# Performance work log

Hardware: AMD Instinct MI355X
Metric: run time of the kernel (lower is better)

The kernel has to match this reference:

```python
import jax, jax.numpy as jnp
import numpy as np

B, S, D = 4, 1024, 512
H, HD, M = 8, 64, 2
EPS = 1e-5


def setup_inputs() -> dict:
    key = jax.random.key(0)
    ks = jax.random.split(key, 8)
    scale = 0.02
    x = jax.random.normal(ks[0], (B, S, D), dtype=jnp.float32)
    Wq = jax.random.normal(ks[1], (D, D), dtype=jnp.float32) * scale
    Wk = jax.random.normal(ks[2], (D, D), dtype=jnp.float32) * scale
    Wv = jax.random.normal(ks[3], (D, D), dtype=jnp.float32) * scale
    Wo = jax.random.normal(ks[4], (D, D), dtype=jnp.float32) * scale
    bo = jnp.zeros((D,), dtype=jnp.float32)
    Wg = jax.random.normal(ks[5], (H * (2 + M), D), dtype=jnp.float32) * scale
    bg = jnp.zeros((H * (2 + M),), dtype=jnp.float32)
    init_decays = jnp.array([0.95, 0.8], dtype=jnp.float32)
    logit = jnp.log(init_decays / (1.0 - init_decays))
    logit_alphas = jnp.tile(logit[None, :], (H, 1))  # [H, M]
    ln_w = jnp.ones((D,), dtype=jnp.float32)
    ln_b = jnp.zeros((D,), dtype=jnp.float32)
    return {"x": x, "Wq": Wq, "Wk": Wk, "Wv": Wv, "Wo": Wo, "bo": bo,
            "Wg": Wg, "bg": bg, "logit_alphas": logit_alphas,
            "ln_w": ln_w, "ln_b": ln_b}


def _rope(x):
    # x: [B, S, H, HD] interleaved rotary
    half = HD // 2
    inv_freq = 1.0 / (10000.0 ** (jnp.arange(half, dtype=jnp.float32) / half))
    t = jnp.arange(S, dtype=jnp.float32)
    freqs = t[:, None] * inv_freq[None, :]            # [S, half]
    cos = jnp.cos(freqs)[None, :, None, :]            # [1, S, 1, half]
    sin = jnp.sin(freqs)[None, :, None, :]
    x1, x2 = x[..., ::2], x[..., 1::2]
    o1 = x1 * cos - x2 * sin
    o2 = x1 * sin + x2 * cos
    return jnp.stack((o1, o2), axis=-1).reshape(x.shape)


def _forward(x, Wq, Wk, Wv, Wo, bo, Wg, bg, logit_alphas, ln_w, ln_b):
    residual = x
    q = (x @ Wq.T).reshape(B, S, H, HD)
    k = (x @ Wk.T).reshape(B, S, H, HD)
    v = (x @ Wv.T).reshape(B, S, H, HD)
    q = _rope(q)
    k = _rope(k)

    gates = (x @ Wg.T + bg).reshape(B, S, H, 2 + M)
    g_f = jax.nn.sigmoid(gates[..., 0])               # [B, S, H]
    g_u = jax.nn.sigmoid(gates[..., 1])               # [B, S, H]
    w_mix = jax.nn.softmax(gates[..., 2:], axis=-1)   # [B, S, H, M]
    alphas = jax.nn.sigmoid(logit_alphas)             # [H, M]

    # time-major for scan
    qs = jnp.moveaxis(q, 1, 0)       # [S, B, H, HD]
    ks = jnp.moveaxis(k, 1, 0)
    vs = jnp.moveaxis(v, 1, 0)
    gfs = jnp.moveaxis(g_f, 1, 0)    # [S, B, H]
    gus = jnp.moveaxis(g_u, 1, 0)
    wms = jnp.moveaxis(w_mix, 1, 0)  # [S, B, H, M]

    state0 = jnp.zeros((B, H, M, HD, HD), dtype=x.dtype)

    def step(state, inp):
        qt, kt, vt, gf, gu, wt = inp
        retain = alphas[None, :, :] * gf[:, :, None]           # [B, H, M]
        write_w = wt * gu[..., None]                           # [B, H, M]
        outer = jnp.einsum('bhd,bhe->bhde', kt, vt)            # [B, H, HD, HD]
        state = (state * retain[..., None, None]
                 + outer[:, :, None, :, :] * write_w[..., None, None])
        S_read = jnp.einsum('bhmde,bhm->bhde', state, wt)      # [B, H, HD, HD]
        o = jnp.einsum('bhd,bhde->bhe', qt, S_read)            # [B, H, HD]
        return state, o

    _, outs = jax.lax.scan(step, state0, (qs, ks, vs, gfs, gus, wms))
    out = jnp.moveaxis(outs, 0, 1).reshape(B, S, H * HD)
    out = out @ Wo.T + bo
    y = residual + out
    mu = jnp.mean(y, axis=-1, keepdims=True)
    var = jnp.mean(jnp.square(y - mu), axis=-1, keepdims=True)
    return (y - mu) / jnp.sqrt(var + EPS) * ln_w + ln_b


def reference(x, Wq, Wk, Wv, Wo, bo, Wg, bg, logit_alphas, ln_w, ln_b):
    return _forward(x, Wq, Wk, Wv, Wo, bo, Wg, bg, logit_alphas, ln_w, ln_b)
```

## Files before the change

kernel.cpp:

```cpp
#include <hip/hip_runtime.h>
#include <hip/hip_bf16.h>
#include <math.h>

#define B_  4
#define S_  1024
#define D_  512
#define H_  8
#define HD_ 64
#define EPS_ 1e-5f

typedef __attribute__((ext_vector_type(8))) short  bf16x8;
typedef __attribute__((ext_vector_type(4))) short  bf16x4;
typedef __attribute__((ext_vector_type(4))) float  f32x4;

#define MFMA16(a, b, c) __builtin_amdgcn_mfma_f32_16x16x32_bf16((a), (b), (c), 0, 0, 0)

#define GLOAD16(gp, lp) __builtin_amdgcn_global_load_lds( \
    (const __attribute__((address_space(1))) unsigned int*)(gp), \
    (__attribute__((address_space(3))) unsigned int*)(lp), 16, 0, 0)

__device__ __forceinline__ float bf2f(short u) {
    union { unsigned int i; float f; } v;
    v.i = ((unsigned int)(unsigned short)u) << 16;
    return v.f;
}
__device__ __forceinline__ short f2bf(float f) {
    __hip_bfloat16 h = __float2bfloat16(f);
    return *reinterpret_cast<short*>(&h);
}

__global__ __launch_bounds__(256) void convert_inputs(
    const float* __restrict__ x,
    const float* __restrict__ Wq, const float* __restrict__ Wk,
    const float* __restrict__ Wv, const float* __restrict__ Wg,
    const float* __restrict__ Wo,
    short* __restrict__ xbf, short* __restrict__ Wcat, short* __restrict__ Wobf,
    float2* __restrict__ rope)
{
    const int id = blockIdx.x * 256 + threadIdx.x;
    if (id < 262144) {
        const size_t e = (size_t)id * 8;
        float4 v0 = *(const float4*)(x + e);
        float4 v1 = *(const float4*)(x + e + 4);
        bf16x8 o = { f2bf(v0.x), f2bf(v0.y), f2bf(v0.z), f2bf(v0.w),
                     f2bf(v1.x), f2bf(v1.y), f2bf(v1.z), f2bf(v1.w) };
        *(bf16x8*)(xbf + e) = o;
    } else if (id < 368640) {
        const int i2 = id - 262144;
        const int row = i2 >> 6;
        const int c8 = (i2 & 63) * 8;
        const float* s = nullptr;
        if (row < 512)       s = Wq + (size_t)row * 512 + c8;
        else if (row < 1024) s = Wk + (size_t)(row - 512) * 512 + c8;
        else if (row < 1536) s = Wv + (size_t)(row - 1024) * 512 + c8;
        else if (row < 1568) s = Wg + (size_t)(row - 1536) * 512 + c8;
        bf16x8 o = (bf16x8)0;
        if (s) {
            float4 v0 = *(const float4*)(s);
            float4 v1 = *(const float4*)(s + 4);
            o = bf16x8{ f2bf(v0.x), f2bf(v0.y), f2bf(v0.z), f2bf(v0.w),
                        f2bf(v1.x), f2bf(v1.y), f2bf(v1.z), f2bf(v1.w) };
        }
        *(bf16x8*)(Wcat + (size_t)row * 512 + c8) = o;
    } else if (id < 401408) {
        const int i3 = id - 368640;
        const size_t e = (size_t)i3 * 8;
        float4 v0 = *(const float4*)(Wo + e);
        float4 v1 = *(const float4*)(Wo + e + 4);
        bf16x8 o = { f2bf(v0.x), f2bf(v0.y), f2bf(v0.z), f2bf(v0.w),
                     f2bf(v1.x), f2bf(v1.y), f2bf(v1.z), f2bf(v1.w) };
        *(bf16x8*)(Wobf + e) = o;
    } else {
        const int i4 = id - 401408;
        const int s = i4 >> 5, i = i4 & 31;
        const float inv = exp2f(-(float)i * (13.287712379549449f / 32.0f));
        float sn, cs;
        sincosf((float)s * inv, &sn, &cs);
        rope[i4] = make_float2(cs, sn);
    }
}

__global__ __launch_bounds__(256) void mfma_proj(
    const short* __restrict__ Abf, const short* __restrict__ Wcat,
    const float2* __restrict__ rope,
    short* __restrict__ Qbf, short* __restrict__ Kbf,
    short* __restrict__ Vbf, float* __restrict__ Graw)
{
    __shared__ __align__(16) short lds[32768];

    const int p = blockIdx.x;
    const int xcd = p & 7, slot = p >> 3;
    const int by = xcd + 8 * (slot / 13);
    const int bx = slot % 13;
    const int n0 = bx * 128, m0 = by * 128;

    const int tid = threadIdx.x;
    const int lane = tid & 63, wave = tid >> 6;
    const int lrow = lane & 15, lgrp = lane >> 4;
    const int wr = wave >> 1, wc = wave & 1;
    const int srl = lane >> 3;
    const int scs = (lane & 7) * 8;

    f32x4 acc[4][4];
    #pragma unroll
    for (int i = 0; i < 4; ++i)
        #pragma unroll
        for (int j = 0; j < 4; ++j) acc[i][j] = (f32x4)0.f;

    #define PROJ_STAGE(buf, kt)  {                                            \
        short* dA = lds + (buf) * 16384;                                      \
        short* dB = dA + 8192;                                                \
        _Pragma("unroll")                                                     \
        for (int i = 0; i < 4; ++i) {                                         \
            const int chunk = i * 4 + wave;                                   \
            const int r = chunk * 8 + srl;                                    \
            GLOAD16(Abf  + (size_t)(m0 + r) * 512 + (kt) + scs, dA + chunk * 512); \
            GLOAD16(Wcat + (size_t)(n0 + r) * 512 + (kt) + scs, dB + chunk * 512); \
        } }

    PROJ_STAGE(0, 0);
    __syncthreads();
    int cur = 0;
    for (int step = 0; step < 8; ++step) {
        if (step < 7) PROJ_STAGE(cur ^ 1, (step + 1) * 64);
        const short* sA = lds + cur * 16384;
        const short* sB = sA + 8192;
        #pragma unroll
        for (int kk = 0; kk < 2; ++kk) {
            const int kb = kk * 32 + lgrp * 8;
            bf16x8 af[4], bfr[4];
            #pragma unroll
            for (int mi = 0; mi < 4; ++mi)
                af[mi] = *(const bf16x8*)&sA[(wr * 64 + mi * 16 + lrow) * 64 + kb];
            #pragma unroll
            for (int ni = 0; ni < 4; ++ni)
                bfr[ni] = *(const bf16x8*)&sB[(wc * 64 + ni * 16 + lrow) * 64 + kb];
            #pragma unroll
            for (int mi = 0; mi < 4; ++mi)
                #pragma unroll
                for (int ni = 0; ni < 4; ++ni)
                    acc[mi][ni] = MFMA16(af[mi], bfr[ni], acc[mi][ni]);
        }
        __syncthreads();
        cur ^= 1;
    }
    #undef PROJ_STAGE

    if (n0 < 1536) {
        short* stg = lds;
        #pragma unroll
        for (int mi = 0; mi < 4; ++mi)
            #pragma unroll
            for (int ni = 0; ni < 4; ++ni)
                #pragma unroll
                for (int j = 0; j < 4; ++j) {
                    const int rl = wr * 64 + mi * 16 + lgrp * 4 + j;
                    const int cl = wc * 64 + ni * 16 + lrow;
                    stg[rl * 136 + cl] = f2bf(acc[mi][ni][j]);
                }
        __syncthreads();
        short* dst; int dstoff; bool roped;
        if (n0 < 512)       { dst = Qbf; dstoff = n0;        roped = true;  }
        else if (n0 < 1024) { dst = Kbf; dstoff = n0 - 512;  roped = true;  }
        else                { dst = Vbf; dstoff = n0 - 1024; roped = false; }
        #pragma unroll
        for (int it = 0; it < 8; ++it) {
            const int c8 = tid + it * 256;
            const int row = c8 >> 4, co = (c8 & 15) * 8;
            bf16x8 vv = *(const bf16x8*)&stg[row * 136 + co];
            if (roped) {
                const int s = (m0 + row) & (S_ - 1);
                const int ib = ((dstoff + co) & 63) >> 1;
                #pragma unroll
                for (int j = 0; j < 4; ++j) {
                    const float2 t = rope[s * 32 + ib + j];
                    const float xr = bf2f(vv[2 * j]), xi = bf2f(vv[2 * j + 1]);
                    vv[2 * j]     = f2bf(xr * t.x - xi * t.y);
                    vv[2 * j + 1] = f2bf(xr * t.y + xi * t.x);
                }
            }
            *(bf16x8*)(dst + (size_t)(m0 + row) * 512 + dstoff + co) = vv;
        }
    } else {
        #pragma unroll
        for (int mi = 0; mi < 4; ++mi)
            #pragma unroll
            for (int ni = 0; ni < 2; ++ni) {
                const int col = wc * 64 + ni * 16 + lrow;
                if (col < 32) {
                    #pragma unroll
                    for (int j = 0; j < 4; ++j) {
                        const int row = m0 + wr * 64 + mi * 16 + lgrp * 4 + j;
                        Graw[(size_t)row * 32 + col] = acc[mi][ni][j];
                    }
                }
            }
    }
}

__global__ __launch_bounds__(256) void chunk_delta(
    const short* __restrict__ Kbf, const short* __restrict__ Vbf,
    const float* __restrict__ Graw, const float* __restrict__ bg,
    const float* __restrict__ logit_alphas,
    short* __restrict__ Ubuf, float* __restrict__ SRb)
{
    __shared__ __align__(16) short sK [64 * 72];
    __shared__ __align__(16) short sVT[64 * 72];
    __shared__ __align__(16) short sKscT[2][64 * 72];
    __shared__ float sScal[64][4];
    __shared__ float sKs[2][64];

    const int tid  = threadIdx.x;
    const int wave = tid >> 6, lane = tid & 63;
    const int lrow = lane & 15, lgrp = lane >> 4;
    const int c  = blockIdx.x & 15;
    const int bh = blockIdx.x >> 4;
    const int h = bh & 7, b = bh >> 3;
    const int row0 = wave * 16;
    const int s0 = c * 64;

    if (tid < 64) {
        const int bs = b * S_ + s0 + tid;
        const float4 gv = *(const float4*)(Graw + (size_t)bs * 32 + h * 4);
        const float g0 = gv.x + bg[h * 4 + 0];
        const float g1 = gv.y + bg[h * 4 + 1];
        const float g2 = gv.z + bg[h * 4 + 2];
        const float g3 = gv.w + bg[h * 4 + 3];
        const float gf  = 1.f / (1.f + expf(-g0));
        const float gu  = 1.f / (1.f + expf(-g1));
        const float wm0 = 1.f / (1.f + expf(-(g2 - g3)));
        const float a0 = 1.f / (1.f + expf(-logit_alphas[h * 2 + 0]));
        const float a1 = 1.f / (1.f + expf(-logit_alphas[h * 2 + 1]));
        sScal[tid][0] = a0 * gf; sScal[tid][1] = a1 * gf;
        sScal[tid][2] = wm0 * gu; sScal[tid][3] = (1.f - wm0) * gu;
    }

    #pragma unroll
    for (int it = 0; it < 2; ++it) {
        const int i = tid + it * 256;
        const int r = i >> 3, c8 = (i & 7) * 8;
        const size_t g = ((size_t)(b * S_ + s0 + r)) * 512 + h * 64 + c8;
        bf16x8 k8 = *(const bf16x8*)(Kbf + g);
        bf16x8 v8 = *(const bf16x8*)(Vbf + g);
        *(bf16x8*)&sK[r * 72 + c8] = k8;
        #pragma unroll
        for (int j = 0; j < 8; ++j) sVT[(c8 + j) * 72 + r] = v8[j];
    }
    __syncthreads();

    if (wave < 2) {
        const int m = wave;
        float pre = log2f(sScal[lane][m]);
        #pragma unroll
        for (int off = 1; off < 64; off <<= 1) {
            const float u = __shfl_up(pre, off);
            if (lane >= off) pre += u;
        }
        const float lR = __shfl(pre, 63);
        sKs[m][lane] = sScal[lane][2 + m] * exp2f(lR - pre);
        if (lane == 63) SRb[blockIdx.x * 2 + m] = exp2f(lR);
    }
    __syncthreads();

    {
        const int task = tid >> 1, halfd = tid & 1;
        const int m = task >> 6, tau = task & 63;
        const float ksc = sKs[m][tau];
        #pragma unroll
        for (int dd = halfd * 32; dd < halfd * 32 + 32; dd += 8) {
            bf16x8 kr = *(const bf16x8*)&sK[tau * 72 + dd];
            #pragma unroll
            for (int j = 0; j < 8; ++j)
                sKscT[m][(dd + j) * 72 + tau] = f2bf(bf2f(kr[j]) * ksc);
        }
    }
    __syncthreads();

    #pragma unroll
    for (int m = 0; m < 2; ++m) {
        f32x4 accU[4];
        #pragma unroll
        for (int db = 0; db < 4; ++db) accU[db] = (f32x4)0.f;
        #pragma unroll
        for (int kk = 0; kk < 2; ++kk) {
            const int kb = kk * 32 + lgrp * 8;
            bf16x8 a = *(const bf16x8*)&sVT[(row0 + lrow) * 72 + kb];
            #pragma unroll
            for (int db = 0; db < 4; ++db) {
                bf16x8 bb = *(const bf16x8*)&sKscT[m][(db * 16 + lrow) * 72 + kb];
                accU[db] = MFMA16(a, bb, accU[db]);
            }
        }
        __syncthreads();
        #pragma unroll
        for (int db = 0; db < 4; ++db)
            #pragma unroll
            for (int r = 0; r < 4; ++r) {
                const int e = row0 + lgrp * 4 + r;
                sK[e * 72 + db * 16 + lrow] = f2bf(accU[db][r]);
            }
        __syncthreads();
        short* ub = Ubuf + ((size_t)blockIdx.x * 2 + m) * 4096;
        #pragma unroll
        for (int it = 0; it < 2; ++it) {
            const int i = tid + it * 256;
            const int e = i >> 3, seg = (i & 7) * 8;
            *(bf16x8*)(ub + e * 64 + seg) = *(const bf16x8*)&sK[e * 72 + seg];
        }
    }
}

__global__ __launch_bounds__(256) void chunk_o(
    const short* __restrict__ Qbf, const short* __restrict__ Kbf,
    const short* __restrict__ Vbf, const float* __restrict__ Graw,
    const float* __restrict__ bg, const float* __restrict__ logit_alphas,
    const short* __restrict__ Ubuf, const float* __restrict__ SRb,
    short* __restrict__ Obf)
{
    __shared__ __align__(16) short sQ [64 * 72];
    __shared__ __align__(16) short sK [64 * 72];
    __shared__ __align__(16) short sVT[64 * 72];
    __shared__ __align__(16) short sP [64 * 72];
    __shared__ __align__(16) short sST[2][64 * 72];
    __shared__ float sScal[64][6];
    __shared__ float sLc[2][64];
    __shared__ float sQs[2][64];

    const int tid  = threadIdx.x;
    const int wave = tid >> 6, lane = tid & 63;
    const int lrow = lane & 15, lgrp = lane >> 4;
    const int c  = blockIdx.x & 15;
    const int bh = blockIdx.x >> 4;
    const int h = bh & 7, b = bh >> 3;
    const int row0 = wave * 16;
    const int s0 = c * 64;

    if (tid < 64) {
        const int bs = b * S_ + s0 + tid;
        const float4 gv = *(const float4*)(Graw + (size_t)bs * 32 + h * 4);
        const float g0 = gv.x + bg[h * 4 + 0];
        const float g1 = gv.y + bg[h * 4 + 1];
        const float g2 = gv.z + bg[h * 4 + 2];
        const float g3 = gv.w + bg[h * 4 + 3];
        const float gf  = 1.f / (1.f + expf(-g0));
        const float gu  = 1.f / (1.f + expf(-g1));
        const float wm0 = 1.f / (1.f + expf(-(g2 - g3)));
        const float a0 = 1.f / (1.f + expf(-logit_alphas[h * 2 + 0]));
        const float a1 = 1.f / (1.f + expf(-logit_alphas[h * 2 + 1]));
        sScal[tid][0] = a0 * gf; sScal[tid][1] = a1 * gf;
        sScal[tid][2] = wm0 * gu; sScal[tid][3] = (1.f - wm0) * gu;
        sScal[tid][4] = wm0; sScal[tid][5] = 1.f - wm0;
    }

    float sp[4][8];
    #pragma unroll
    for (int g = 0; g < 4; ++g)
        #pragma unroll
        for (int j = 0; j < 8; ++j) sp[g][j] = 0.f;
    for (int cp = 0; cp < c; ++cp) {
        const int bhc = bh * 16 + cp;
        const float R0 = SRb[bhc * 2 + 0];
        const float R1 = SRb[bhc * 2 + 1];
        const short* ub = Ubuf + (size_t)bhc * 8192;
        #pragma unroll
        for (int g = 0; g < 4; ++g) {
            bf16x8 u = *(const bf16x8*)(ub + g * 2048 + tid * 8);
            const float R = (g < 2) ? R0 : R1;
            #pragma unroll
            for (int j = 0; j < 8; ++j) sp[g][j] = fmaf(R, sp[g][j], bf2f(u[j]));
        }
    }
    #pragma unroll
    for (int g = 0; g < 4; ++g) {
        const int i = g * 2048 + tid * 8;
        const int m = i >> 12, e = (i >> 6) & 63, d = i & 63;
        bf16x8 o;
        #pragma unroll
        for (int j = 0; j < 8; ++j) o[j] = f2bf(sp[g][j]);
        *(bf16x8*)&sST[m][e * 72 + d] = o;
    }

    #pragma unroll
    for (int it = 0; it < 2; ++it) {
        const int i = tid + it * 256;
        const int r = i >> 3, c8 = (i & 7) * 8;
        const size_t g = ((size_t)(b * S_ + s0 + r)) * 512 + h * 64 + c8;
        *(bf16x8*)&sQ[r * 72 + c8] = *(const bf16x8*)(Qbf + g);
        *(bf16x8*)&sK[r * 72 + c8] = *(const bf16x8*)(Kbf + g);
        bf16x8 v8 = *(const bf16x8*)(Vbf + g);
        #pragma unroll
        for (int j = 0; j < 8; ++j) sVT[(c8 + j) * 72 + r] = v8[j];
    }
    __syncthreads();

    if (wave < 2) {
        const int m = wave;
        float pre = log2f(sScal[lane][m]);
        #pragma unroll
        for (int off = 1; off < 64; off <<= 1) {
            const float u = __shfl_up(pre, off);
            if (lane >= off) pre += u;
        }
        sLc[m][lane] = pre;
        sQs[m][lane] = sScal[lane][4 + m] * exp2f(pre);
    }
    __syncthreads();

    f32x4 accS[4], accO[4];
    #pragma unroll
    for (int cb = 0; cb < 4; ++cb) { accS[cb] = (f32x4)0.f; accO[cb] = (f32x4)0.f; }
    #pragma unroll
    for (int kk = 0; kk < 2; ++kk) {
        const int kb = kk * 32 + lgrp * 8;
        bf16x8 a = *(const bf16x8*)&sQ[(row0 + lrow) * 72 + kb];
        #pragma unroll
        for (int cb = 0; cb < 4; ++cb) {
            bf16x8 bb = *(const bf16x8*)&sK[(cb * 16 + lrow) * 72 + kb];
            accS[cb] = MFMA16(a, bb, accS[cb]);
        }
    }

    #pragma unroll
    for (int kk = 0; kk < 4; ++kk) {
        const int k0 = kk * 32 + lgrp * 8;
        const int m = k0 >> 6, d0 = k0 & 63;
        const float qs = sQs[m][row0 + lrow];
        bf16x8 qr = *(const bf16x8*)&sQ[(row0 + lrow) * 72 + d0];
        bf16x8 a;
        #pragma unroll
        for (int j = 0; j < 8; ++j) a[j] = f2bf(bf2f(qr[j]) * qs);
        #pragma unroll
        for (int cb = 0; cb < 4; ++cb) {
            bf16x8 bb = *(const bf16x8*)&sST[m][(cb * 16 + lrow) * 72 + d0];
            accO[cb] = MFMA16(a, bb, accO[cb]);
        }
    }

    #pragma unroll
    for (int r = 0; r < 4; ++r) {
        const int t = row0 + lgrp * 4 + r;
        const float wm0 = sScal[t][4], wm1 = sScal[t][5];
        const float lc0t = sLc[0][t],  lc1t = sLc[1][t];
        #pragma unroll
        for (int cb = 0; cb < 4; ++cb) {
            const int tau = cb * 16 + lrow;
            float p = 0.f;
            if (tau <= t) {
                const float c0 = wm0 * sScal[tau][2] * exp2f(lc0t - sLc[0][tau]);
                const float c1 = wm1 * sScal[tau][3] * exp2f(lc1t - sLc[1][tau]);
                p = accS[cb][r] * (c0 + c1);
            }
            sP[t * 72 + tau] = f2bf(p);
        }
    }

    #pragma unroll
    for (int kk = 0; kk < 2; ++kk) {
        const int kb = kk * 32 + lgrp * 8;
        bf16x8 a = *(const bf16x8*)&sP[(row0 + lrow) * 72 + kb];
        #pragma unroll
        for (int cb = 0; cb < 4; ++cb) {
            bf16x8 bb = *(const bf16x8*)&sVT[(cb * 16 + lrow) * 72 + kb];
            accO[cb] = MFMA16(a, bb, accO[cb]);
        }
    }

    #pragma unroll
    for (int cb = 0; cb < 4; ++cb)
        #pragma unroll
        for (int r = 0; r < 4; ++r) {
            const int t = row0 + lgrp * 4 + r;
            sP[t * 72 + cb * 16 + lrow] = f2bf(accO[cb][r]);
        }
    __syncthreads();
    #pragma unroll
    for (int it = 0; it < 2; ++it) {
        const int i = tid + it * 256;
        const int t = i >> 3, seg = (i & 7) * 8;
        *(bf16x8*)(Obf + ((size_t)(b * S_ + s0 + t)) * 512 + h * 64 + seg) =
            *(const bf16x8*)&sP[t * 72 + seg];
    }
}

__global__ __launch_bounds__(256) void mfma_out(
    const short* __restrict__ Abf, const short* __restrict__ Wobf,
    const float* __restrict__ bo, const float* __restrict__ xres,
    short* __restrict__ Ybf)
{
    __shared__ __align__(16) short lds[24576];

    const int p = blockIdx.x;
    const int xcd = p & 7, slot = p >> 3;
    const int by = xcd + 8 * (slot >> 3);
    const int bx = slot & 7;
    const int n0 = bx * 64, m0 = by * 128;

    const int tid = threadIdx.x;
    const int lane = tid & 63, wave = tid >> 6;
    const int lrow = lane & 15, lgrp = lane >> 4;
    const int wr = wave >> 1, wc = wave & 1;
    const int srl = lane >> 3;
    const int scs = (lane & 7) * 8;

    f32x4 acc[4][2];
    #pragma unroll
    for (int i = 0; i < 4; ++i)
        #pragma unroll
        for (int j = 0; j < 2; ++j) acc[i][j] = (f32x4)0.f;

    #define OUT_STAGE(buf, kt)  {                                             \
        short* dA = lds + (buf) * 12288;                                      \
        short* dB = dA + 8192;                                                \
        _Pragma("unroll")                                                     \
        for (int i = 0; i < 4; ++i) {                                         \
            const int chunk = i * 4 + wave;                                   \
            const int r = chunk * 8 + srl;                                    \
            GLOAD16(Abf + (size_t)(m0 + r) * 512 + (kt) + scs, dA + chunk * 512); \
        }                                                                     \
        _Pragma("unroll")                                                     \
        for (int i = 0; i < 2; ++i) {                                         \
            const int chunk = i * 4 + wave;                                   \
            const int r = chunk * 8 + srl;                                    \
            GLOAD16(Wobf + (size_t)(n0 + r) * 512 + (kt) + scs, dB + chunk * 512); \
        } }

    OUT_STAGE(0, 0);
    __syncthreads();
    int cur = 0;
    for (int step = 0; step < 8; ++step) {
        if (step < 7) OUT_STAGE(cur ^ 1, (step + 1) * 64);
        const short* sA = lds + cur * 12288;
        const short* sB = sA + 8192;
        #pragma unroll
        for (int kk = 0; kk < 2; ++kk) {
            const int kb = kk * 32 + lgrp * 8;
            bf16x8 af[4], bfr[2];
            #pragma unroll
            for (int mi = 0; mi < 4; ++mi)
                af[mi] = *(const bf16x8*)&sA[(wr * 64 + mi * 16 + lrow) * 64 + kb];
            #pragma unroll
            for (int ni = 0; ni < 2; ++ni)
                bfr[ni] = *(const bf16x8*)&sB[(wc * 32 + ni * 16 + lrow) * 64 + kb];
            #pragma unroll
            for (int mi = 0; mi < 4; ++mi)
                #pragma unroll
                for (int ni = 0; ni < 2; ++ni)
                    acc[mi][ni] = MFMA16(af[mi], bfr[ni], acc[mi][ni]);
        }
        __syncthreads();
        cur ^= 1;
    }
    #undef OUT_STAGE

    short* stg = lds;
    #pragma unroll
    for (int mi = 0; mi < 4; ++mi)
        #pragma unroll
        for (int ni = 0; ni < 2; ++ni)
            #pragma unroll
            for (int j = 0; j < 4; ++j) {
                const int rl = wr * 64 + mi * 16 + lgrp * 4 + j;
                const int cl = wc * 32 + ni * 16 + lrow;
                stg[rl * 80 + cl] = f2bf(acc[mi][ni][j]);
            }
    __syncthreads();
    #pragma unroll
    for (int it = 0; it < 4; ++it) {
        const int u = tid + it * 256;
        const int row = u >> 3, seg = (u & 7) * 8;
        const size_t gbase = (size_t)(m0 + row) * 512 + n0 + seg;
        bf16x8 a = *(const bf16x8*)&stg[row * 80 + seg];
        float4 x0 = *(const float4*)(xres + gbase);
        float4 x1 = *(const float4*)(xres + gbase + 4);
        float4 b0 = *(const float4*)(bo + n0 + seg);
        float4 b1 = *(const float4*)(bo + n0 + seg + 4);
        bf16x8 y;
        y[0] = f2bf(bf2f(a[0]) + b0.x + x0.x);
        y[1] = f2bf(bf2f(a[1]) + b0.y + x0.y);
        y[2] = f2bf(bf2f(a[2]) + b0.z + x0.z);
        y[3] = f2bf(bf2f(a[3]) + b0.w + x0.w);
        y[4] = f2bf(bf2f(a[4]) + b1.x + x1.x);
        y[5] = f2bf(bf2f(a[5]) + b1.y + x1.y);
        y[6] = f2bf(bf2f(a[6]) + b1.z + x1.z);
        y[7] = f2bf(bf2f(a[7]) + b1.w + x1.w);
        *(bf16x8*)(Ybf + gbase) = y;
    }
}

__global__ __launch_bounds__(256) void ln_kernel(
    const short* __restrict__ Ybf, const float* __restrict__ ln_w,
    const float* __restrict__ ln_b, float* __restrict__ out)
{
    const int wave = threadIdx.x >> 6;
    const int lane = threadIdx.x & 63;
    const int row = blockIdx.x * 4 + wave;

    bf16x8 v8 = *(const bf16x8*)(Ybf + (size_t)row * 512 + lane * 8);
    float v[8];
    #pragma unroll
    for (int j = 0; j < 8; ++j) v[j] = bf2f(v8[j]);

    float s = 0.f, sq = 0.f;
    #pragma unroll
    for (int j = 0; j < 8; ++j) { s += v[j]; sq += v[j] * v[j]; }
    #pragma unroll
    for (int off = 32; off; off >>= 1) {
        s  += __shfl_xor(s,  off);
        sq += __shfl_xor(sq, off);
    }
    const float mu  = s * (1.f / 512.f);
    const float var = sq * (1.f / 512.f) - mu * mu;
    const float inv = rsqrtf(var + EPS_);

    float4 w0 = *(const float4*)(ln_w + lane * 8);
    float4 w1 = *(const float4*)(ln_w + lane * 8 + 4);
    float4 b0 = *(const float4*)(ln_b + lane * 8);
    float4 b1 = *(const float4*)(ln_b + lane * 8 + 4);
    float4 o0, o1;
    o0.x = (v[0] - mu) * inv * w0.x + b0.x;
    o0.y = (v[1] - mu) * inv * w0.y + b0.y;
    o0.z = (v[2] - mu) * inv * w0.z + b0.z;
    o0.w = (v[3] - mu) * inv * w0.w + b0.w;
    o1.x = (v[4] - mu) * inv * w1.x + b1.x;
    o1.y = (v[5] - mu) * inv * w1.y + b1.y;
    o1.z = (v[6] - mu) * inv * w1.z + b1.z;
    o1.w = (v[7] - mu) * inv * w1.w + b1.w;
    *(float4*)(out + (size_t)row * 512 + lane * 8)     = o0;
    *(float4*)(out + (size_t)row * 512 + lane * 8 + 4) = o1;
}

extern "C" void kernel_launch(void* const* d_in, const int* in_sizes, int n_in,
                              void* d_out, int out_size, void* d_ws, size_t ws_size,
                              hipStream_t stream)
{
    const float* x   = (const float*)d_in[0];
    const float* Wq  = (const float*)d_in[1];
    const float* Wk  = (const float*)d_in[2];
    const float* Wv  = (const float*)d_in[3];
    const float* Wo  = (const float*)d_in[4];
    const float* bo  = (const float*)d_in[5];
    const float* Wg  = (const float*)d_in[6];
    const float* bg  = (const float*)d_in[7];
    const float* la  = (const float*)d_in[8];
    const float* lnw = (const float*)d_in[9];
    const float* lnb = (const float*)d_in[10];

    const size_t NQ = (size_t)B_ * S_ * D_;
    float* Graw = (float*)d_ws;
    float* ROPE = Graw + 131072;
    float* SRb  = ROPE + 65536;
    short* xbf  = (short*)(SRb + 1024);
    short* Wcat = xbf + NQ;
    short* Wobf = Wcat + (size_t)1664 * 512;
    short* Qbf  = Wobf + (size_t)512 * 512;
    short* Kbf  = Qbf + NQ;
    short* Vbf  = Kbf + NQ;
    short* Obf  = Vbf + NQ;
    short* Ybf  = Obf + NQ;
    short* Ubuf = Ybf + NQ;

    convert_inputs<<<1696, 256, 0, stream>>>(x, Wq, Wk, Wv, Wg, Wo, xbf, Wcat, Wobf,
                                             (float2*)ROPE);
    mfma_proj<<<416, 256, 0, stream>>>(xbf, Wcat, (const float2*)ROPE,
                                       Qbf, Kbf, Vbf, Graw);
    chunk_delta<<<512, 256, 0, stream>>>(Kbf, Vbf, Graw, bg, la, Ubuf, SRb);
    chunk_o<<<512, 256, 0, stream>>>(Qbf, Kbf, Vbf, Graw, bg, la, Ubuf, SRb, Obf);
    mfma_out<<<256, 256, 0, stream>>>(Obf, Wobf, bo, x, Ybf);
    ln_kernel<<<1024, 256, 0, stream>>>(Ybf, lnw, lnb, (float*)d_out);
}
```

Baseline: 131.1 us.

## Fuse QKV/gate projection with per-chunk delta computation into one kernel

```diff
diff --git a/kernel.cpp b/kernel.cpp
--- a/kernel.cpp
+++ b/kernel.cpp
@@ -10,7 +10,6 @@
 #define EPS_ 1e-5f
 
 typedef __attribute__((ext_vector_type(8))) short  bf16x8;
-typedef __attribute__((ext_vector_type(4))) short  bf16x4;
 typedef __attribute__((ext_vector_type(4))) float  f32x4;
 
 #define MFMA16(a, b, c) __builtin_amdgcn_mfma_f32_16x16x32_bf16((a), (b), (c), 0, 0, 0)
@@ -80,135 +79,224 @@
     }
 }
 
-__global__ __launch_bounds__(256) void mfma_proj(
-    const short* __restrict__ Abf, const short* __restrict__ Wcat,
-    const float2* __restrict__ rope,
-    short* __restrict__ Qbf, short* __restrict__ Kbf,
-    short* __restrict__ Vbf, float* __restrict__ Graw)
+__global__ __launch_bounds__(256) void proj_scan_a(
+    const short* __restrict__ xbf, const short* __restrict__ Wcat,
+    const float2* __restrict__ rope, const float* __restrict__ bg,
+    const float* __restrict__ logit_alphas,
+    short* __restrict__ Qbf, short* __restrict__ Kbf, short* __restrict__ Vbf,
+    short* __restrict__ Ubuf, float* __restrict__ SRb, float* __restrict__ SCAL)
 {
-    __shared__ __align__(16) short lds[32768];
-
-    const int p = blockIdx.x;
-    const int xcd = p & 7, slot = p >> 3;
-    const int by = xcd + 8 * (slot / 13);
-    const int bx = slot % 13;
-    const int n0 = bx * 128, m0 = by * 128;
+    __shared__ __align__(16) char smem[58368];
+    short* sQ   = (short*)(smem);
+    short* sK   = (short*)(smem + 9216);
+    short* sVT  = (short*)(smem + 18432);
+    short* sP   = (short*)(smem + 27648);
+    short* sSTb = (short*)(smem + 36864);
+    float (*sScal)[6] = (float(*)[6])(smem + 55296);
+    float* sKs  = (float*)(smem + 56832);
+    float* sG   = (float*)(smem + 57344);
+    short* Bstage = sQ;
+    short* Astage = sSTb;
 
     const int tid = threadIdx.x;
-    const int lane = tid & 63, wave = tid >> 6;
+    const int wave = tid >> 6, lane = tid & 63;
     const int lrow = lane & 15, lgrp = lane >> 4;
-    const int wr = wave >> 1, wc = wave & 1;
+    const int c  = blockIdx.x & 15;
+    const int bh = blockIdx.x >> 4;
+    const int h = bh & 7, b = bh >> 3;
+    const int s0 = c * 64;
+    const int row0 = wave * 16;
     const int srl = lane >> 3;
     const int scs = (lane & 7) * 8;
 
-    f32x4 acc[4][4];
-    #pragma unroll
-    for (int i = 0; i < 4; ++i)
-        #pragma unroll
-        for (int j = 0; j < 4; ++j) acc[i][j] = (f32x4)0.f;
-
-    #define PROJ_STAGE(buf, kt)  {                                            \
-        short* dA = lds + (buf) * 16384;                                      \
-        short* dB = dA + 8192;                                                \
-        _Pragma("unroll")                                                     \
-        for (int i = 0; i < 4; ++i) {                                         \
-            const int chunk = i * 4 + wave;                                   \
-            const int r = chunk * 8 + srl;                                    \
-            GLOAD16(Abf  + (size_t)(m0 + r) * 512 + (kt) + scs, dA + chunk * 512); \
-            GLOAD16(Wcat + (size_t)(n0 + r) * 512 + (kt) + scs, dB + chunk * 512); \
-        } }
-
-    PROJ_STAGE(0, 0);
-    __syncthreads();
-    int cur = 0;
+    f32x4 acc[13];
+    #pragma unroll
+    for (int n = 0; n < 13; ++n) acc[n] = (f32x4)0.f;
+
     for (int step = 0; step < 8; ++step) {
-        if (step < 7) PROJ_STAGE(cur ^ 1, (step + 1) * 64);
-        const short* sA = lds + cur * 16384;
-        const short* sB = sA + 8192;
+        const int kt = step * 64;
+        #pragma unroll
+        for (int i = 0; i < 2; ++i) {
+            const int ch = wave * 2 + i;
+            const size_t gr = (size_t)(b * S_ + s0 + ch * 8 + srl) * 512 + kt + scs;
+            GLOAD16(xbf + gr, Astage + ch * 512);
+        }
+        #pragma unroll
+        for (int i = 0; i < 7; ++i) {
+            const int ch = i * 4 + wave;
+            if (ch < 26) {
+                int grow;
+                if (ch < 8)       grow = h * 64 + ch * 8;
+                else if (ch < 16) grow = 512 + h * 64 + (ch - 8) * 8;
+                else if (ch < 24) grow = 1024 + h * 64 + (ch - 16) * 8;
+                else              grow = 1536 + h * 4 + (ch - 24) * 8;
+                GLOAD16(Wcat + (size_t)(grow + srl) * 512 + kt + scs, Bstage + ch * 512);
+            }
+        }
+        __syncthreads();
         #pragma unroll
         for (int kk = 0; kk < 2; ++kk) {
             const int kb = kk * 32 + lgrp * 8;
-            bf16x8 af[4], bfr[4];
-            #pragma unroll
-            for (int mi = 0; mi < 4; ++mi)
-                af[mi] = *(const bf16x8*)&sA[(wr * 64 + mi * 16 + lrow) * 64 + kb];
-            #pragma unroll
-            for (int ni = 0; ni < 4; ++ni)
-                bfr[ni] = *(const bf16x8*)&sB[(wc * 64 + ni * 16 + lrow) * 64 + kb];
-            #pragma unroll
-            for (int mi = 0; mi < 4; ++mi)
-                #pragma unroll
-                for (int ni = 0; ni < 4; ++ni)
-                    acc[mi][ni] = MFMA16(af[mi], bfr[ni], acc[mi][ni]);
+            bf16x8 a = *(const bf16x8*)&Astage[(row0 + lrow) * 64 + kb];
+            #pragma unroll
+            for (int n = 0; n < 13; ++n) {
+                bf16x8 bb = *(const bf16x8*)&Bstage[(n * 16 + lrow) * 64 + kb];
+                acc[n] = MFMA16(a, bb, acc[n]);
+            }
         }
         __syncthreads();
-        cur ^= 1;
-    }
-    #undef PROJ_STAGE
-
-    if (n0 < 1536) {
-        short* stg = lds;
-        #pragma unroll
-        for (int mi = 0; mi < 4; ++mi)
-            #pragma unroll
-            for (int ni = 0; ni < 4; ++ni)
-                #pragma unroll
-                for (int j = 0; j < 4; ++j) {
-                    const int rl = wr * 64 + mi * 16 + lgrp * 4 + j;
-                    const int cl = wc * 64 + ni * 16 + lrow;
-                    stg[rl * 136 + cl] = f2bf(acc[mi][ni][j]);
-                }
+    }
+
+    #pragma unroll
+    for (int n = 0; n < 4; ++n)
+        #pragma unroll
+        for (int j = 0; j < 4; ++j) {
+            const int r = row0 + lgrp * 4 + j;
+            sQ[r * 72 + n * 16 + lrow]    = f2bf(acc[n][j]);
+            sK[r * 72 + n * 16 + lrow]    = f2bf(acc[4 + n][j]);
+            const short vb = f2bf(acc[8 + n][j]);
+            sVT[(n * 16 + lrow) * 72 + r] = vb;
+            sP [r * 72 + n * 16 + lrow]   = vb;
+        }
+    if (lrow < 4)
+        #pragma unroll
+        for (int j = 0; j < 4; ++j)
+            sG[(row0 + lgrp * 4 + j) * 4 + lrow] = acc[12][j];
+    __syncthreads();
+
+    if (tid < 64) {
+        const float g0 = sG[tid * 4 + 0] + bg[h * 4 + 0];
+        const float g1 = sG[tid * 4 + 1] + bg[h * 4 + 1];
+        const float g2 = sG[tid * 4 + 2] + bg[h * 4 + 2];
+        const float g3 = sG[tid * 4 + 3] + bg[h * 4 + 3];
+        const float gf  = 1.f / (1.f + expf(-g0));
+        const float gu  = 1.f / (1.f + expf(-g1));
+        const float wm0 = 1.f / (1.f + expf(-(g2 - g3)));
+        const float a0 = 1.f / (1.f + expf(-logit_alphas[h * 2 + 0]));
+        const float a1 = 1.f / (1.f + expf(-logit_alphas[h * 2 + 1]));
+        sScal[tid][0] = a0 * gf; sScal[tid][1] = a1 * gf;
+        sScal[tid][2] = wm0 * gu; sScal[tid][3] = (1.f - wm0) * gu;
+        sScal[tid][4] = wm0; sScal[tid][5] = 1.f - wm0;
+    }
+    #pragma unroll
+    for (int it = 0; it < 2; ++it) {
+        const int i = tid + it * 256;
+        const int r = i >> 3, c8 = (i & 7) * 8;
+        const int s = s0 + r;
+        bf16x8 q8 = *(const bf16x8*)&sQ[r * 72 + c8];
+        bf16x8 k8 = *(const bf16x8*)&sK[r * 72 + c8];
+        bf16x8 qo, ko;
+        #pragma unroll
+        for (int j = 0; j < 4; ++j) {
+            const float2 t = rope[s * 32 + (c8 >> 1) + j];
+            const float qx = bf2f(q8[2 * j]), qy = bf2f(q8[2 * j + 1]);
+            const float kx = bf2f(k8[2 * j]), ky = bf2f(k8[2 * j + 1]);
+            qo[2 * j]     = f2bf(qx * t.x - qy * t.y);
+            qo[2 * j + 1] = f2bf(qx * t.y + qy * t.x);
+            ko[2 * j]     = f2bf(kx * t.x - ky * t.y);
+            ko[2 * j + 1] = f2bf(kx * t.y + ky * t.x);
+        }
+        *(bf16x8*)&sQ[r * 72 + c8] = qo;
+        *(bf16x8*)&sK[r * 72 + c8] = ko;
+    }
+    #pragma unroll
+    for (int it = 0; it < 2; ++it) {
+        const int i = tid + it * 256;
+        const int r = i >> 3, seg = (i & 7) * 8;
+        *(bf16x8*)(Vbf + ((size_t)(b * S_ + s0 + r)) * 512 + h * 64 + seg) =
+            *(const bf16x8*)&sP[r * 72 + seg];
+    }
+    __syncthreads();
+
+    if (wave < 2) {
+        const int m = wave;
+        float pre = log2f(sScal[lane][m]);
+        #pragma unroll
+        for (int off = 1; off < 64; off <<= 1) {
+            const float u = __shfl_up(pre, off);
+            if (lane >= off) pre += u;
+        }
+        const float lR = __shfl(pre, 63);
+        sKs[m * 64 + lane] = sScal[lane][2 + m] * exp2f(lR - pre);
+        float* sc = SCAL + ((size_t)(bh * S_) + s0 + lane) * 8;
+        sc[0 + m] = pre;
+        sc[2 + m] = sScal[lane][2 + m];
+        sc[4 + m] = sScal[lane][4 + m];
+        sc[6 + m] = sScal[lane][4 + m] * exp2f(pre);
+        if (lane == 63) SRb[blockIdx.x * 2 + m] = exp2f(lR);
+    }
+    #pragma unroll
+    for (int it = 0; it < 2; ++it) {
+        const int i = tid + it * 256;
+        const int r = i >> 3, seg = (i & 7) * 8;
+        const size_t g = ((size_t)(b * S_ + s0 + r)) * 512 + h * 64 + seg;
+        *(bf16x8*)(Qbf + g) = *(const bf16x8*)&sQ[r * 72 + seg];
+        *(bf16x8*)(Kbf + g) = *(const bf16x8*)&sK[r * 72 + seg];
+    }
+    __syncthreads();
+
+    {
+        const int task = tid >> 1, halfd = tid & 1;
+        const int m = task >> 6, tau = task & 63;
+        short* kt_ = sSTb + m * 4608;
+        const float ksc = sKs[m * 64 + tau];
+        #pragma unroll
+        for (int dd = halfd * 32; dd < halfd * 32 + 32; dd += 8) {
+            bf16x8 kr = *(const bf16x8*)&sK[tau * 72 + dd];
+            #pragma unroll
+            for (int j = 0; j < 8; ++j)
+                kt_[(dd + j) * 72 + tau] = f2bf(bf2f(kr[j]) * ksc);
+        }
+    }
+    __syncthreads();
+
+    #pragma unroll
+    for (int m = 0; m < 2; ++m) {
+        f32x4 accU[4];
+        #pragma unroll
+        for (int db = 0; db < 4; ++db) accU[db] = (f32x4)0.f;
+        const short* kt_ = sSTb + m * 4608;
+        #pragma unroll
+        for (int kk = 0; kk < 2; ++kk) {
+            const int kb = kk * 32 + lgrp * 8;
+            bf16x8 a = *(const bf16x8*)&sVT[(row0 + lrow) * 72 + kb];
+            #pragma unroll
+            for (int db = 0; db < 4; ++db) {
+                bf16x8 bb = *(const bf16x8*)&kt_[(db * 16 + lrow) * 72 + kb];
+                accU[db] = MFMA16(a, bb, accU[db]);
+            }
+        }
         __syncthreads();
-        short* dst; int dstoff; bool roped;
-        if (n0 < 512)       { dst = Qbf; dstoff = n0;        roped = true;  }
-        else if (n0 < 1024) { dst = Kbf; dstoff = n0 - 512;  roped = true;  }
-        else                { dst = Vbf; dstoff = n0 - 1024; roped = false; }
-        #pragma unroll
-        for (int it = 0; it < 8; ++it) {
-            const int c8 = tid + it * 256;
-            const int row = c8 >> 4, co = (c8 & 15) * 8;
-            bf16x8 vv = *(const bf16x8*)&stg[row * 136 + co];
-            if (roped) {
-                const int s = (m0 + row) & (S_ - 1);
-                const int ib = ((dstoff + co) & 63) >> 1;
-                #pragma unroll
-                for (int j = 0; j < 4; ++j) {
-                    const float2 t = rope[s * 32 + ib + j];
-                    const float xr = bf2f(vv[2 * j]), xi = bf2f(vv[2 * j + 1]);
-                    vv[2 * j]     = f2bf(xr * t.x - xi * t.y);
-                    vv[2 * j + 1] = f2bf(xr * t.y + xi * t.x);
-                }
+        #pragma unroll
+        for (int db = 0; db < 4; ++db)
+            #pragma unroll
+            for (int r = 0; r < 4; ++r) {
+                const int e = row0 + lgrp * 4 + r;
+                sP[e * 72 + db * 16 + lrow] = f2bf(accU[db][r]);
             }
-            *(bf16x8*)(dst + (size_t)(m0 + row) * 512 + dstoff + co) = vv;
-        }
-    } else {
-        #pragma unroll
-        for (int mi = 0; mi < 4; ++mi)
-            #pragma unroll
-            for (int ni = 0; ni < 2; ++ni) {
-                const int col = wc * 64 + ni * 16 + lrow;
-                if (col < 32) {
-                    #pragma unroll
-                    for (int j = 0; j < 4; ++j) {
-                        const int row = m0 + wr * 64 + mi * 16 + lgrp * 4 + j;
-                        Graw[(size_t)row * 32 + col] = acc[mi][ni][j];
-                    }
-                }
-            }
-    }
-}
-
-__global__ __launch_bounds__(256) void chunk_delta(
-    const short* __restrict__ Kbf, const short* __restrict__ Vbf,
-    const float* __restrict__ Graw, const float* __restrict__ bg,
-    const float* __restrict__ logit_alphas,
-    short* __restrict__ Ubuf, float* __restrict__ SRb)
+        __syncthreads();
+        short* ub = Ubuf + ((size_t)blockIdx.x * 2 + m) * 4096;
+        #pragma unroll
+        for (int it = 0; it < 2; ++it) {
+            const int i = tid + it * 256;
+            const int e = i >> 3, seg = (i & 7) * 8;
+            *(bf16x8*)(ub + e * 64 + seg) = *(const bf16x8*)&sP[e * 72 + seg];
+        }
+    }
+}
+
+__global__ __launch_bounds__(256) void chunk_o(
+    const short* __restrict__ Qbf, const short* __restrict__ Kbf,
+    const short* __restrict__ Vbf, const float* __restrict__ SCAL,
+    const short* __restrict__ Ubuf, const float* __restrict__ SRb,
+    short* __restrict__ Obf)
 {
+    __shared__ __align__(16) short sQ [64 * 72];
     __shared__ __align__(16) short sK [64 * 72];
     __shared__ __align__(16) short sVT[64 * 72];
-    __shared__ __align__(16) short sKscT[2][64 * 72];
-    __shared__ float sScal[64][4];
-    __shared__ float sKs[2][64];
+    __shared__ __align__(16) short sP [64 * 72];
+    __shared__ __align__(16) short sST[2][64 * 72];
+    __shared__ float sScal[64][8];
 
     const int tid  = threadIdx.x;
     const int wave = tid >> 6, lane = tid & 63;
@@ -220,136 +308,9 @@
     const int s0 = c * 64;
 
     if (tid < 64) {
-        const int bs = b * S_ + s0 + tid;
-        const float4 gv = *(const float4*)(Graw + (size_t)bs * 32 + h * 4);
-        const float g0 = gv.x + bg[h * 4 + 0];
-        const float g1 = gv.y + bg[h * 4 + 1];
-        const float g2 = gv.z + bg[h * 4 + 2];
-        const float g3 = gv.w + bg[h * 4 + 3];
-        const float gf  = 1.f / (1.f + expf(-g0));
-        const float gu  = 1.f / (1.f + expf(-g1));
-        const float wm0 = 1.f / (1.f + expf(-(g2 - g3)));
-        const float a0 = 1.f / (1.f + expf(-logit_alphas[h * 2 + 0]));
-        const float a1 = 1.f / (1.f + expf(-logit_alphas[h * 2 + 1]));
-        sScal[tid][0] = a0 * gf; sScal[tid][1] = a1 * gf;
-        sScal[tid][2] = wm0 * gu; sScal[tid][3] = (1.f - wm0) * gu;
-    }
-
-    #pragma unroll
-    for (int it = 0; it < 2; ++it) {
-        const int i = tid + it * 256;
-        const int r = i >> 3, c8 = (i & 7) * 8;
-        const size_t g = ((size_t)(b * S_ + s0 + r)) * 512 + h * 64 + c8;
-        bf16x8 k8 = *(const bf16x8*)(Kbf + g);
-        bf16x8 v8 = *(const bf16x8*)(Vbf + g);
-        *(bf16x8*)&sK[r * 72 + c8] = k8;
-        #pragma unroll
-        for (int j = 0; j < 8; ++j) sVT[(c8 + j) * 72 + r] = v8[j];
-    }
-    __syncthreads();
-
-    if (wave < 2) {
-        const int m = wave;
-        float pre = log2f(sScal[lane][m]);
-        #pragma unroll
-        for (int off = 1; off < 64; off <<= 1) {
-            const float u = __shfl_up(pre, off);
-            if (lane >= off) pre += u;
-        }
-        const float lR = __shfl(pre, 63);
-        sKs[m][lane] = sScal[lane][2 + m] * exp2f(lR - pre);
-        if (lane == 63) SRb[blockIdx.x * 2 + m] = exp2f(lR);
-    }
-    __syncthreads();
-
-    {
-        const int task = tid >> 1, halfd = tid & 1;
-        const int m = task >> 6, tau = task & 63;
-        const float ksc = sKs[m][tau];
-        #pragma unroll
-        for (int dd = halfd * 32; dd < halfd * 32 + 32; dd += 8) {
-            bf16x8 kr = *(const bf16x8*)&sK[tau * 72 + dd];
-            #pragma unroll
-            for (int j = 0; j < 8; ++j)
-                sKscT[m][(dd + j) * 72 + tau] = f2bf(bf2f(kr[j]) * ksc);
-        }
-    }
-    __syncthreads();
-
-    #pragma unroll
-    for (int m = 0; m < 2; ++m) {
-        f32x4 accU[4];
-        #pragma unroll
-        for (int db = 0; db < 4; ++db) accU[db] = (f32x4)0.f;
-        #pragma unroll
-        for (int kk = 0; kk < 2; ++kk) {
-            const int kb = kk * 32 + lgrp * 8;
-            bf16x8 a = *(const bf16x8*)&sVT[(row0 + lrow) * 72 + kb];
-            #pragma unroll
-            for (int db = 0; db < 4; ++db) {
-                bf16x8 bb = *(const bf16x8*)&sKscT[m][(db * 16 + lrow) * 72 + kb];
-                accU[db] = MFMA16(a, bb, accU[db]);
-            }
-        }
-        __syncthreads();
-        #pragma unroll
-        for (int db = 0; db < 4; ++db)
-            #pragma unroll
-            for (int r = 0; r < 4; ++r) {
-                const int e = row0 + lgrp * 4 + r;
-                sK[e * 72 + db * 16 + lrow] = f2bf(accU[db][r]);
-            }
-        __syncthreads();
-        short* ub = Ubuf + ((size_t)blockIdx.x * 2 + m) * 4096;
-        #pragma unroll
-        for (int it = 0; it < 2; ++it) {
-            const int i = tid + it * 256;
-            const int e = i >> 3, seg = (i & 7) * 8;
-            *(bf16x8*)(ub + e * 64 + seg) = *(const bf16x8*)&sK[e * 72 + seg];
-        }
-    }
-}
-
-__global__ __launch_bounds__(256) void chunk_o(
-    const short* __restrict__ Qbf, const short* __restrict__ Kbf,
-    const short* __restrict__ Vbf, const float* __restrict__ Graw,
-    const float* __restrict__ bg, const float* __restrict__ logit_alphas,
-    const short* __restrict__ Ubuf, const float* __restrict__ SRb,
-    short* __restrict__ Obf)
-{
-    __shared__ __align__(16) short sQ [64 * 72];
-    __shared__ __align__(16) short sK [64 * 72];
-    __shared__ __align__(16) short sVT[64 * 72];
-    __shared__ __align__(16) short sP [64 * 72];
-    __shared__ __align__(16) short sST[2][64 * 72];
-    __shared__ float sScal[64][6];
-    __shared__ float sLc[2][64];
-    __shared__ float sQs[2][64];
-
-    const int tid  = threadIdx.x;
-    const int wave = tid >> 6, lane = tid & 63;
-    const int lrow = lane & 15, lgrp = lane >> 4;
-    const int c  = blockIdx.x & 15;
-    const int bh = blockIdx.x >> 4;
-    const int h = bh & 7, b = bh >> 3;
-    const int row0 = wave * 16;
-    const int s0 = c * 64;
-
-    if (tid < 64) {
-        const int bs = b * S_ + s0 + tid;
-        const float4 gv = *(const float4*)(Graw + (size_t)bs * 32 + h * 4);
-        const float g0 = gv.x + bg[h * 4 + 0];
-        const float g1 = gv.y + bg[h * 4 + 1];
-        const float g2 = gv.z + bg[h * 4 + 2];
-        const float g3 = gv.w + bg[h * 4 + 3];
-        const float gf  = 1.f / (1.f + expf(-g0));
-        const float gu  = 1.f / (1.f + expf(-g1));
-        const float wm0 = 1.f / (1.f + expf(-(g2 - g3)));
-        const float a0 = 1.f / (1.f + expf(-logit_alphas[h * 2 + 0]));
-        const float a1 = 1.f / (1.f + expf(-logit_alphas[h * 2 + 1]));
-        sScal[tid][0] = a0 * gf; sScal[tid][1] = a1 * gf;
-        sScal[tid][2] = wm0 * gu; sScal[tid][3] = (1.f - wm0) * gu;
-        sScal[tid][4] = wm0; sScal[tid][5] = 1.f - wm0;
+        const float* sc = SCAL + ((size_t)(bh * S_) + s0 + tid) * 8;
+        *(float4*)&sScal[tid][0] = *(const float4*)sc;
+        *(float4*)&sScal[tid][4] = *(const float4*)(sc + 4);
     }
 
     float sp[4][8];
@@ -393,19 +354,6 @@
     }
     __syncthreads();
 
-    if (wave < 2) {
-        const int m = wave;
-        float pre = log2f(sScal[lane][m]);
-        #pragma unroll
-        for (int off = 1; off < 64; off <<= 1) {
-            const float u = __shfl_up(pre, off);
-            if (lane >= off) pre += u;
-        }
-        sLc[m][lane] = pre;
-        sQs[m][lane] = sScal[lane][4 + m] * exp2f(pre);
-    }
-    __syncthreads();
-
     f32x4 accS[4], accO[4];
     #pragma unroll
     for (int cb = 0; cb < 4; ++cb) { accS[cb] = (f32x4)0.f; accO[cb] = (f32x4)0.f; }
@@ -424,7 +372,7 @@
     for (int kk = 0; kk < 4; ++kk) {
         const int k0 = kk * 32 + lgrp * 8;
         const int m = k0 >> 6, d0 = k0 & 63;
-        const float qs = sQs[m][row0 + lrow];
+        const float qs = sScal[row0 + lrow][6 + m];
         bf16x8 qr = *(const bf16x8*)&sQ[(row0 + lrow) * 72 + d0];
         bf16x8 a;
         #pragma unroll
@@ -440,14 +388,14 @@
     for (int r = 0; r < 4; ++r) {
         const int t = row0 + lgrp * 4 + r;
         const float wm0 = sScal[t][4], wm1 = sScal[t][5];
-        const float lc0t = sLc[0][t],  lc1t = sLc[1][t];
+        const float lc0t = sScal[t][0], lc1t = sScal[t][1];
         #pragma unroll
         for (int cb = 0; cb < 4; ++cb) {
             const int tau = cb * 16 + lrow;
             float p = 0.f;
             if (tau <= t) {
-                const float c0 = wm0 * sScal[tau][2] * exp2f(lc0t - sLc[0][tau]);
-                const float c1 = wm1 * sScal[tau][3] * exp2f(lc1t - sLc[1][tau]);
+                const float c0 = wm0 * sScal[tau][2] * exp2f(lc0t - sScal[tau][0]);
+                const float c1 = wm1 * sScal[tau][3] * exp2f(lc1t - sScal[tau][1]);
                 p = accS[cb][r] * (c0 + c1);
             }
             sP[t * 72 + tau] = f2bf(p);
@@ -646,10 +594,10 @@
     const float* lnb = (const float*)d_in[10];
 
     const size_t NQ = (size_t)B_ * S_ * D_;
-    float* Graw = (float*)d_ws;
-    float* ROPE = Graw + 131072;
+    float* ROPE = (float*)d_ws;
     float* SRb  = ROPE + 65536;
-    short* xbf  = (short*)(SRb + 1024);
+    float* SCAL = SRb + 1024;
+    short* xbf  = (short*)(SCAL + 262144);
     short* Wcat = xbf + NQ;
     short* Wobf = Wcat + (size_t)1664 * 512;
     short* Qbf  = Wobf + (size_t)512 * 512;
@@ -661,10 +609,9 @@
 
     convert_inputs<<<1696, 256, 0, stream>>>(x, Wq, Wk, Wv, Wg, Wo, xbf, Wcat, Wobf,
                                              (float2*)ROPE);
-    mfma_proj<<<416, 256, 0, stream>>>(xbf, Wcat, (const float2*)ROPE,
-                                       Qbf, Kbf, Vbf, Graw);
-    chunk_delta<<<512, 256, 0, stream>>>(Kbf, Vbf, Graw, bg, la, Ubuf, SRb);
-    chunk_o<<<512, 256, 0, stream>>>(Qbf, Kbf, Vbf, Graw, bg, la, Ubuf, SRb, Obf);
+    proj_scan_a<<<512, 256, 0, stream>>>(xbf, Wcat, (const float2*)ROPE, bg, la,
+                                         Qbf, Kbf, Vbf, Ubuf, SRb, SCAL);
+    chunk_o<<<512, 256, 0, stream>>>(Qbf, Kbf, Vbf, SCAL, Ubuf, SRb, Obf);
     mfma_out<<<256, 256, 0, stream>>>(Obf, Wobf, bo, x, Ybf);
     ln_kernel<<<1024, 256, 0, stream>>>(Ybf, lnw, lnb, (float*)d_out);
 }
```

Result: no change. 132.7 us (+1.2%).
